# Kernel optimization log

Measured on AMD Instinct MI355X. Metric: run time of the kernel, lower is better.

Reference implementation:

```python
import jax, jax.numpy as jnp
import numpy as np
from jax import lax

B, T, N, H, NC = 2, 8, 512, 64, 10
NEG = -1e9
LN_EPS = 1e-5


def _gatv2(x, mask, Wl, Wr, att, b):
    # GATv2Conv (PyG semantics, eval mode): e_ij = att . leaky_relu(Wr x_i + Wl x_j),
    # softmax over source nodes j with self-loops, out_i = sum_j alpha_ij * (Wl x_j).
    # x: (B, N, Fin); mask: (N, N) bool adjacency incl. self-loops; att: (heads, C).
    heads, C = att.shape
    Bn, Nn, _ = x.shape
    xl = (x @ Wl).reshape(Bn, Nn, heads, C)  # source transform
    xr = (x @ Wr).reshape(Bn, Nn, heads, C)  # target transform
    s = jax.nn.leaky_relu(xr[:, :, None] + xl[:, None, :], 0.2)  # (B, Ni, Nj, h, C)
    e = jnp.einsum('bijhc,hc->bijh', s, att)
    e = jnp.where(mask[None, :, :, None], e, NEG)
    alpha = jax.nn.softmax(e, axis=2)  # softmax over neighbors j
    out = jnp.einsum('bijh,bjhc->bihc', alpha, xl)
    return out.reshape(Bn, Nn, heads * C) + b


def _gru_layer(x, Wih, Whh, bih, bhh):
    # torch nn.GRU single layer, batch_first; x: (B, T, Hin)
    h0 = jnp.zeros((x.shape[0], Whh.shape[0]), x.dtype)
    def step(h, xt):
        gi = xt @ Wih + bih
        gh = h @ Whh + bhh
        ir, iz, inn = jnp.split(gi, 3, axis=-1)
        hr, hz, hn = jnp.split(gh, 3, axis=-1)
        r = jax.nn.sigmoid(ir + hr)
        z = jax.nn.sigmoid(iz + hz)
        n = jnp.tanh(inn + r * hn)
        hnew = (1.0 - z) * n + z * h
        return hnew, hnew
    _, ys = lax.scan(step, h0, jnp.swapaxes(x, 0, 1))
    return jnp.swapaxes(ys, 0, 1)


def setup_inputs() -> dict:
    key = jax.random.key(0)
    ks = jax.random.split(key, 20)
    def rn(i, shape, s=0.1):
        return jax.random.normal(ks[i], shape, jnp.float32) * s
    x_seq = jax.random.normal(ks[0], (B, T, N, 1), jnp.float32)
    a = jax.random.uniform(ks[1], (N, N))
    up = jnp.triu((a > 0.95).astype(jnp.float32), 1)
    static_adj = up + up.T  # sparse symmetric 0/1 static graph
    dyn_W = jax.random.normal(ks[2], (N, N), jnp.float32)
    reg_lambda = jnp.array([0.05], jnp.float32)
    return {
        'x_seq': x_seq, 'static_adj': static_adj, 'dyn_W': dyn_W, 'reg_lambda': reg_lambda,
        'g1_Wl': rn(3, (1, H)), 'g1_Wr': rn(4, (1, H)), 'g1_att': rn(5, (4, H // 4)), 'g1_b': jnp.zeros(H),
        'g2_Wl': rn(6, (H, H)), 'g2_Wr': rn(7, (H, H)), 'g2_att': rn(8, (1, H)), 'g2_b': jnp.zeros(H),
        'gru_Wih0': rn(9, (H, 3 * H)), 'gru_Whh0': rn(10, (H, 3 * H)), 'gru_bih0': jnp.zeros(3 * H), 'gru_bhh0': jnp.zeros(3 * H),
        'gru_Wih1': rn(11, (H, 3 * H)), 'gru_Whh1': rn(12, (H, 3 * H)), 'gru_bih1': jnp.zeros(3 * H), 'gru_bhh1': jnp.zeros(3 * H),
        'attn_W': rn(13, (H, 1)), 'attn_b': jnp.zeros(1),
        'cls_W1': rn(14, (H, H)), 'cls_b1': jnp.zeros(H), 'ln_g': jnp.ones(H), 'ln_b': jnp.zeros(H),
        'cls_W2': rn(15, (H, NC)), 'cls_b2': jnp.zeros(NC),
    }


def reference(x_seq, static_adj, dyn_W, reg_lambda,
              g1_Wl, g1_Wr, g1_att, g1_b, g2_Wl, g2_Wr, g2_att, g2_b,
              gru_Wih0, gru_Whh0, gru_bih0, gru_bhh0,
              gru_Wih1, gru_Whh1, gru_bih1, gru_bhh1,
              attn_W, attn_b, cls_W1, cls_b1, ln_g, ln_b, cls_W2, cls_b2):
    Bn, Tn, Nn, _ = x_seq.shape
    lam = jnp.maximum(reg_lambda[0], 0.01)
    t = jnp.arange(Tn, dtype=x_seq.dtype)
    gts = jnp.exp(-lam * t)  # gating values per timestep
    dyn = jax.nn.relu(dyn_W + dyn_W.T)
    fused = gts[:, None, None] * static_adj + (1.0 - gts)[:, None, None] * dyn  # (T, N, N)
    masks = (fused > 0) | jnp.eye(Nn, dtype=bool)[None]  # edge set + self-loops

    def step(carry, inp):
        xt, mask = inp  # xt: (B, N, 1)
        h = jax.nn.elu(_gatv2(xt, mask, g1_Wl, g1_Wr, g1_att, g1_b))
        h = jax.nn.elu(_gatv2(h, mask, g2_Wl, g2_Wr, g2_att, g2_b))
        return carry, h.mean(axis=1)  # (B, H) graph readout

    _, reps = lax.scan(step, 0.0, (jnp.swapaxes(x_seq, 0, 1), masks))
    h_seq = jnp.swapaxes(reps, 0, 1)  # (B, T, H)

    gru_out = _gru_layer(h_seq, gru_Wih0, gru_Whh0, gru_bih0, gru_bhh0)
    gru_out = _gru_layer(gru_out, gru_Wih1, gru_Whh1, gru_bih1, gru_bhh1)

    att_scores = jax.nn.softmax((gru_out @ attn_W + attn_b)[..., 0], axis=1)  # (B, T)
    final = jnp.einsum('bt,bth->bh', att_scores, gru_out)

    z = final @ cls_W1 + cls_b1
    mu = jnp.mean(z, axis=-1, keepdims=True)
    var = jnp.var(z, axis=-1, keepdims=True)
    z = (z - mu) / jnp.sqrt(var + LN_EPS) * ln_g + ln_b
    z = jax.nn.gelu(z, approximate=False)
    logits = z @ cls_W2 + cls_b2
    return logits, gts, att_scores
```

## Files before the change

kernel.cpp:

```cpp
#include <hip/hip_runtime.h>
#include <math.h>

#define BB 2
#define TT 8
#define NN 512
#define HH 64
#define NC 10

typedef unsigned char uchar;

__device__ __forceinline__ float elu1(float v){ return v > 0.f ? v : expm1f(v); }
__device__ __forceinline__ float sigm(float v){ return 1.f/(1.f+expf(-v)); }

__global__ __launch_bounds__(256) void k_mask(
    const float* __restrict__ dW, const float* __restrict__ sadj,
    uchar* __restrict__ M0, uchar* __restrict__ M1,
    float* __restrict__ Z2, float* __restrict__ hseq,
    const float* __restrict__ att1, const float* __restrict__ Wr1,
    const float* __restrict__ Wl1, float* __restrict__ AB,
    const float* __restrict__ Whh0, const float* __restrict__ Wih1,
    const float* __restrict__ Whh1, float4* __restrict__ WT4)
{
    __shared__ float tr[64][65];
    int bx = blockIdx.x, by = blockIdx.y;
    int tid = threadIdx.x;
    if (blockIdx.z == 1){
        int idx = (by*8 + bx)*256 + tid;
        if (idx < 3*4096){
            int m = idx >> 12, r = idx & 4095;
            int gg = r >> 6, k = r & 63;
            const float* W = (m == 0) ? Whh0 : (m == 1) ? Wih1 : Whh1;
            float4 o;
            o.x = W[k*192 + gg];
            o.y = W[k*192 + 64 + gg];
            o.z = W[k*192 + 128 + gg];
            o.w = 0.f;
            WT4[(size_t)m*4096 + r] = o;
        }
        return;
    }
    int i0 = by*64, j0 = bx*64;
    #pragma unroll
    for (int q = 0; q < 4; ++q){
        int r = (tid >> 4) + 16*q, c4 = tid & 15;
        float4 v = *(const float4*)&dW[(size_t)(j0+r)*NN + i0 + 4*c4];
        tr[r][4*c4+0] = v.x; tr[r][4*c4+1] = v.y;
        tr[r][4*c4+2] = v.z; tr[r][4*c4+3] = v.w;
    }
    __syncthreads();
    #pragma unroll
    for (int q = 0; q < 4; ++q){
        int row = (tid >> 4) + 16*q, c4 = tid & 15;
        int i = i0 + row, j = j0 + 4*c4;
        float4 d  = *(const float4*)&dW[(size_t)i*NN + j];
        float4 sa = *(const float4*)&sadj[(size_t)i*NN + j];
        uchar4 m0, m1;
        float dd0 = d.x + tr[4*c4+0][row];
        float dd1 = d.y + tr[4*c4+1][row];
        float dd2 = d.z + tr[4*c4+2][row];
        float dd3 = d.w + tr[4*c4+3][row];
        m0.x = (sa.x > 0.f) || (i == j+0);
        m0.y = (sa.y > 0.f) || (i == j+1);
        m0.z = (sa.z > 0.f) || (i == j+2);
        m0.w = (sa.w > 0.f) || (i == j+3);
        m1.x = m0.x || (dd0 > 0.f);
        m1.y = m0.y || (dd1 > 0.f);
        m1.z = m0.z || (dd2 > 0.f);
        m1.w = m0.w || (dd3 > 0.f);
        *(uchar4*)&M0[(size_t)i*NN + j] = m0;
        *(uchar4*)&M1[(size_t)i*NN + j] = m1;
    }
    int flat = (by*8 + bx)*256 + tid;
    if (flat < BB*TT*NN) Z2[flat] = 0.f;
    else if (flat < BB*TT*NN + BB*TT*HH) hseq[flat - BB*TT*NN] = 0.f;
    if (bx == 0 && by == 0 && tid < 8){
        int h = tid & 3;
        const float* W = (tid < 4) ? Wr1 : Wl1;
        float s = 0.f;
        for (int c = 0; c < 16; ++c) s += att1[h*16+c]*W[h*16+c];
        AB[tid] = s;
    }
}

__global__ __launch_bounds__(256) void k_gat1f(
    const float* __restrict__ x_seq, const uchar* __restrict__ M0,
    const uchar* __restrict__ M1,
    const float* __restrict__ Wl, const float* __restrict__ Wr,
    const float* __restrict__ att, const float* __restrict__ bias,
    const float* __restrict__ AB,
    const float* __restrict__ Wl2, const float* __restrict__ Wr2,
    const float* __restrict__ att2,
    float* __restrict__ xl2, float* __restrict__ xr2,
    float* __restrict__ ui, float* __restrict__ vj)
{
    __shared__ float x_s[NN];
    __shared__ float S_s[4][4];
    __shared__ float h_s[4][HH];
    __shared__ float Wl2_s[64*64];
    __shared__ float Wr2_s[64*64];
    int bt = blockIdx.y; int t = bt % TT;
    int i0 = blockIdx.x * 4;
    int tid = threadIdx.x;
    int il = tid >> 6, jl = tid & 63;
    int i = i0 + il;
    const uchar* M = t ? M1 : M0;
    ((float2*)x_s)[tid] = ((const float2*)(x_seq + bt*NN))[tid];
    #pragma unroll
    for (int q = 0; q < 4; ++q){
        int idx = q*256 + tid;
        ((float4*)Wl2_s)[idx] = ((const float4*)Wl2)[idx];
        ((float4*)Wr2_s)[idx] = ((const float4*)Wr2)[idx];
    }
    __syncthreads();
    float xi = x_s[i];
    const uchar* Mrow = M + (size_t)i*NN;
    float xj[8], msk[8];
    #pragma unroll
    for (int jj = 0; jj < 8; ++jj){
        int j = jj*64 + jl;
        xj[jj] = x_s[j];
        msk[jj] = Mrow[j] ? 1.f : 0.f;
    }
    float sw[4] = {0,0,0,0}, swx[4] = {0,0,0,0};
    for (int h = 0; h < 4; ++h){
        float acc[8] = {0,0,0,0,0,0,0,0};
        #pragma unroll
        for (int c = 0; c < 16; ++c){
            int hc = h*16 + c;
            float wl = Wl[hc];
            float q  = 0.4f * att[hc];
            float pr = xi * Wr[hc];
            #pragma unroll
            for (int jj = 0; jj < 8; ++jj){
                float s = fmaf(xj[jj], wl, pr);
                acc[jj] = fmaf(q, fabsf(s), acc[jj]);
            }
        }
        float lin = 0.6f * xi * AB[h];
        float al6 = 0.6f * AB[4+h];
        #pragma unroll
        for (int jj = 0; jj < 8; ++jj){
            float e = acc[jj] + fmaf(al6, xj[jj], lin);
            float w = msk[jj] * __expf(e);
            sw[h] += w;
            swx[h] = fmaf(w, xj[jj], swx[h]);
        }
    }
    #pragma unroll
    for (int off = 32; off; off >>= 1){
        #pragma unroll
        for (int h = 0; h < 4; ++h){
            sw[h]  += __shfl_down(sw[h],  off);
            swx[h] += __shfl_down(swx[h], off);
        }
    }
    if (jl == 0){
        #pragma unroll
        for (int h = 0; h < 4; ++h) S_s[il][h] = swx[h] / sw[h];
    }
    __syncthreads();
    {
        int hc = tid & 63, row = tid >> 6;
        float v = S_s[row][hc >> 4] * Wl[hc] + bias[hc];
        h_s[row][hc] = elu1(v);
    }
    __syncthreads();
    {
        int c = tid & 63, row = tid >> 6;
        float al = 0.f, ar = 0.f;
        #pragma unroll 8
        for (int k = 0; k < 64; ++k){
            float hv = h_s[row][k];
            al = fmaf(hv, Wl2_s[k*64 + c], al);
            ar = fmaf(hv, Wr2_s[k*64 + c], ar);
        }
        size_t ridx = (size_t)(bt*NN + i0 + row);
        xl2[ridx*HH + c] = al;
        xr2[ridx*HH + c] = ar;
        float a2 = att2[c];
        float pu = a2 * ar, pv = a2 * al;
        #pragma unroll
        for (int off = 32; off; off >>= 1){
            pu += __shfl_down(pu, off);
            pv += __shfl_down(pv, off);
        }
        if (c == 0){ ui[ridx] = pu; vj[ridx] = pv; }
    }
}

__global__ __launch_bounds__(256) void k_e2(
    const float* __restrict__ xl2, const float* __restrict__ xr2,
    const uchar* __restrict__ M0, const uchar* __restrict__ M1,
    const float* __restrict__ att,
    const float* __restrict__ ui, const float* __restrict__ vj,
    float* __restrict__ WgT, float* __restrict__ Z2)
{
    __shared__ float xrT[64][68];
    __shared__ float xlT[64][68];
    int bt = blockIdx.z, t = bt % TT;
    int i0 = blockIdx.y*64, j0 = blockIdx.x*64;
    int base = bt*NN;
    int tid = threadIdx.x;
    const uchar* M = t ? M1 : M0;
    {
        int r = tid >> 2;
        #pragma unroll
        for (int q = 0; q < 4; ++q){
            int c4 = (tid & 3) + 4*q;
            float4 a = *(const float4*)&xr2[(size_t)(base+i0+r)*HH + 4*c4];
            float4 b = *(const float4*)&xl2[(size_t)(base+j0+r)*HH + 4*c4];
            xrT[4*c4+0][r] = a.x; xrT[4*c4+1][r] = a.y;
            xrT[4*c4+2][r] = a.z; xrT[4*c4+3][r] = a.w;
            xlT[4*c4+0][r] = b.x; xlT[4*c4+1][r] = b.y;
            xlT[4*c4+2][r] = b.z; xlT[4*c4+3][r] = b.w;
        }
    }
    int ti = tid >> 4, tj = tid & 15;
    int iL = ti*4, jL = tj*4;
    float4 u4 = *(const float4*)&ui[base+i0+iL];
    float4 v4 = *(const float4*)&vj[base+j0+jL];
    float uu[4] = {u4.x, u4.y, u4.z, u4.w};
    float vv[4] = {v4.x, v4.y, v4.z, v4.w};
    float acc[4][4];
    #pragma unroll
    for (int ii = 0; ii < 4; ++ii)
        #pragma unroll
        for (int jj = 0; jj < 4; ++jj)
            acc[ii][jj] = 0.6f*(uu[ii] + vv[jj]);
    __syncthreads();
    #pragma unroll 8
    for (int c = 0; c < 64; ++c){
        float qa = 0.4f * att[c];
        float4 a4 = *(const float4*)&xrT[c][iL];
        float4 b4 = *(const float4*)&xlT[c][jL];
        float a[4] = {a4.x, a4.y, a4.z, a4.w};
        float b[4] = {b4.x, b4.y, b4.z, b4.w};
        #pragma unroll
        for (int ii = 0; ii < 4; ++ii)
            #pragma unroll
            for (int jj = 0; jj < 4; ++jj)
                acc[ii][jj] = fmaf(qa, fabsf(a[ii] + b[jj]), acc[ii][jj]);
    }
    float w[4][4];
    #pragma unroll
    for (int ii = 0; ii < 4; ++ii){
        int i = i0 + iL + ii;
        uchar4 mr = *(const uchar4*)&M[(size_t)i*NN + j0 + jL];
        w[ii][0] = mr.x ? __expf(acc[ii][0]) : 0.f;
        w[ii][1] = mr.y ? __expf(acc[ii][1]) : 0.f;
        w[ii][2] = mr.z ? __expf(acc[ii][2]) : 0.f;
        w[ii][3] = mr.w ? __expf(acc[ii][3]) : 0.f;
    }
    #pragma unroll
    for (int jj = 0; jj < 4; ++jj){
        int j = j0 + jL + jj;
        float4 wv = { w[0][jj], w[1][jj], w[2][jj], w[3][jj] };
        *(float4*)&WgT[(size_t)(base+j)*NN + i0 + iL] = wv;
    }
    #pragma unroll
    for (int ii = 0; ii < 4; ++ii){
        float zi = w[ii][0] + w[ii][1] + w[ii][2] + w[ii][3];
        zi += __shfl_down(zi, 8);
        zi += __shfl_down(zi, 4);
        zi += __shfl_down(zi, 2);
        zi += __shfl_down(zi, 1);
        if (tj == 0) atomicAdd(&Z2[base + i0 + iL + ii], zi);
    }
}

__global__ __launch_bounds__(256) void k_a2(
    const float* __restrict__ WgT, const float* __restrict__ xl2,
    const float* __restrict__ Z2, const float* __restrict__ bias,
    float* __restrict__ hseq)
{
    __shared__ float a_s[64][20];
    __shared__ float x_s[64][68];
    __shared__ float msum[64];
    int bt = blockIdx.y;
    int i0 = blockIdx.x * 16;
    int base = bt * NN;
    int tid = threadIdx.x;
    int tg = tid >> 4, tc = tid & 15;
    if (tid < 64) msum[tid] = 0.f;
    float4 acc = {0,0,0,0};
    for (int jc = 0; jc < 8; ++jc){
        int j0 = jc*64;
        {
            int row = tid >> 2, c4 = tid & 3;
            ((float4*)&a_s[row][0])[c4] = ((const float4*)&WgT[(size_t)(base+j0+row)*NN + i0])[c4];
        }
        #pragma unroll
        for (int q = 0; q < 4; ++q){
            int idx = q*256 + tid; int row = idx >> 4, c4 = idx & 15;
            ((float4*)&x_s[row][0])[c4] = ((const float4*)&xl2[(size_t)(base+j0+row)*HH])[c4];
        }
        __syncthreads();
        #pragma unroll 8
        for (int j = 0; j < 64; ++j){
            float a = a_s[j][tg];
            float4 xv = ((float4*)&x_s[j][0])[tc];
            acc.x = fmaf(a, xv.x, acc.x);
            acc.y = fmaf(a, xv.y, acc.y);
            acc.z = fmaf(a, xv.z, acc.z);
            acc.w = fmaf(a, xv.w, acc.w);
        }
        __syncthreads();
    }
    float rz = 1.f / Z2[base + i0 + tg];
    float4 b4 = ((const float4*)bias)[tc];
    float4 h;
    h.x = elu1(acc.x*rz + b4.x);
    h.y = elu1(acc.y*rz + b4.y);
    h.z = elu1(acc.z*rz + b4.z);
    h.w = elu1(acc.w*rz + b4.w);
    atomicAdd(&msum[tc*4+0], h.x);
    atomicAdd(&msum[tc*4+1], h.y);
    atomicAdd(&msum[tc*4+2], h.z);
    atomicAdd(&msum[tc*4+3], h.w);
    __syncthreads();
    if (tid < 64) atomicAdd(&hseq[bt*HH + tid], msum[tid]*(1.f/(float)NN));
}

__global__ __launch_bounds__(256) void k_pre(
    const float* __restrict__ hseq, const float* __restrict__ Wih0,
    const float* __restrict__ bih0, float* __restrict__ gi0)
{
    int idx = blockIdx.x*256 + threadIdx.x;
    int bt = idx / 192, g = idx % 192;
    const float* x = hseq + bt*HH;
    float acc = bih0[g];
    #pragma unroll 8
    for (int k = 0; k < HH; ++k)
        acc = fmaf(x[k], Wih0[k*192 + g], acc);
    gi0[idx] = acc;
}

#define P4 65
__global__ __launch_bounds__(512) void k_gru2(
    const float* __restrict__ gi0, const float4* __restrict__ WT4,
    const float* __restrict__ bhh0,
    const float* __restrict__ bih1, const float* __restrict__ bhh1,
    const float* __restrict__ lamp, const float* __restrict__ attn_W,
    const float* __restrict__ attn_b, const float* __restrict__ W1,
    const float* __restrict__ b1, const float* __restrict__ ln_g,
    const float* __restrict__ ln_b, const float* __restrict__ W2,
    const float* __restrict__ b2, float* __restrict__ out)
{
    __shared__ float4 WA[64*P4];
    __shared__ float4 WB[64*P4];
    __shared__ float gi_s[BB*TT*192];
    __shared__ float y_s[BB*TT*HH];
    __shared__ float sc_s[BB][TT], at_s[BB][TT];
    __shared__ float fin_s[BB][HH], z_s[BB][HH], g_s[BB][HH];
    __shared__ float mu_s[BB], iv_s[BB];
    int tid = threadIdx.x;
    int wave = tid >> 6, lane = tid & 63;
    for (int v = tid; v < 4096; v += 512){
        WA[(v >> 6)*P4 + (v & 63)] = WT4[v];
        WB[(v >> 6)*P4 + (v & 63)] = WT4[4096 + v];
    }
    for (int v = tid; v < BB*TT*192; v += 512) gi_s[v] = gi0[v];
    __syncthreads();
    float y[TT];
    float g1r[TT], g1z[TT], g1n[TT];
    if (wave < 2){
        int b = wave;
        float bhr = bhh0[lane], bhz = bhh0[64+lane], bhn = bhh0[128+lane];
        float h = 0.f;
        for (int t = 0; t < TT; ++t){
            float ghr = bhr, ghz = bhz, ghn = bhn;
            #pragma unroll 16
            for (int k = 0; k < 64; ++k){
                float4 w4 = WA[lane*P4 + k];
                float hk = __shfl(h, k);
                ghr = fmaf(w4.x, hk, ghr);
                ghz = fmaf(w4.y, hk, ghz);
                ghn = fmaf(w4.z, hk, ghn);
            }
            const float* gi = &gi_s[(b*TT + t)*192];
            float r = sigm(gi[lane] + ghr);
            float z = sigm(gi[64+lane] + ghz);
            float n = tanhf(gi[128+lane] + r*ghn);
            h = (1.f - z)*n + z*h;
            y[t] = h;
        }
        float bi1r = bih1[lane], bi1z = bih1[64+lane], bi1n = bih1[128+lane];
        #pragma unroll
        for (int t = 0; t < TT; ++t){ g1r[t] = bi1r; g1z[t] = bi1z; g1n[t] = bi1n; }
        #pragma unroll 8
        for (int k = 0; k < 64; ++k){
            float4 w4 = WB[lane*P4 + k];
            #pragma unroll
            for (int t = 0; t < TT; ++t){
                float yk = __shfl(y[t], k);
                g1r[t] = fmaf(w4.x, yk, g1r[t]);
                g1z[t] = fmaf(w4.y, yk, g1z[t]);
                g1n[t] = fmaf(w4.z, yk, g1n[t]);
            }
        }
    }
    __syncthreads();
    if (wave >= 2){
        for (int v = tid - 128; v < 4096; v += 384)
            WA[(v >> 6)*P4 + (v & 63)] = WT4[2*4096 + v];
    }
    __syncthreads();
    if (wave < 2){
        int b = wave;
        float bhr = bhh1[lane], bhz = bhh1[64+lane], bhn = bhh1[128+lane];
        float h = 0.f;
        for (int t = 0; t < TT; ++t){
            float ghr = bhr, ghz = bhz, ghn = bhn;
            #pragma unroll 16
            for (int k = 0; k < 64; ++k){
                float4 w4 = WA[lane*P4 + k];
                float hk = __shfl(h, k);
                ghr = fmaf(w4.x, hk, ghr);
                ghz = fmaf(w4.y, hk, ghz);
                ghn = fmaf(w4.z, hk, ghn);
            }
            float r = sigm(g1r[t] + ghr);
            float z = sigm(g1z[t] + ghz);
            float n = tanhf(g1n[t] + r*ghn);
            h = (1.f - z)*n + z*h;
            y_s[(b*TT + t)*HH + lane] = h;
        }
    }
    __syncthreads();
    float lam = fmaxf(lamp[0], 0.01f);
    if (tid < TT) out[BB*NC + tid] = expf(-lam*(float)tid);
    if (tid < BB*TT){
        int bb = tid >> 3, t = tid & 7;
        float s = attn_b[0];
        const float* r = &y_s[(bb*TT+t)*HH];
        for (int h = 0; h < HH; ++h) s += r[h]*attn_W[h];
        sc_s[bb][t] = s;
    }
    __syncthreads();
    if (tid < BB){
        float mx = -INFINITY;
        for (int t = 0; t < TT; ++t) mx = fmaxf(mx, sc_s[tid][t]);
        float se = 0.f;
        for (int t = 0; t < TT; ++t){ float w = expf(sc_s[tid][t]-mx); at_s[tid][t] = w; se += w; }
        for (int t = 0; t < TT; ++t){
            at_s[tid][t] /= se;
            out[BB*NC + TT + tid*TT + t] = at_s[tid][t];
        }
    }
    __syncthreads();
    if (tid < BB*HH){
        int bb = tid >> 6, h = tid & 63;
        float a = 0.f;
        for (int t = 0; t < TT; ++t) a += at_s[bb][t]*y_s[(bb*TT+t)*HH + h];
        fin_s[bb][h] = a;
    }
    __syncthreads();
    if (tid < BB*HH){
        int bb = tid >> 6, h = tid & 63;
        float a = b1[h];
        for (int k = 0; k < HH; ++k) a += fin_s[bb][k]*W1[k*HH+h];
        z_s[bb][h] = a;
    }
    __syncthreads();
    if (tid < BB){
        float mu = 0.f;
        for (int h = 0; h < HH; ++h) mu += z_s[tid][h];
        mu *= (1.f/HH);
        float v = 0.f;
        for (int h = 0; h < HH; ++h){ float d = z_s[tid][h]-mu; v += d*d; }
        v *= (1.f/HH);
        mu_s[tid] = mu; iv_s[tid] = 1.f/sqrtf(v + 1e-5f);
    }
    __syncthreads();
    if (tid < BB*HH){
        int bb = tid >> 6, h = tid & 63;
        float zn = (z_s[bb][h]-mu_s[bb])*iv_s[bb]*ln_g[h] + ln_b[h];
        g_s[bb][h] = 0.5f*zn*(1.f + erff(zn*0.70710678118654752f));
    }
    __syncthreads();
    if (tid < BB*NC){
        int bb = tid / NC, c = tid % NC;
        float a = b2[c];
        for (int k = 0; k < HH; ++k) a += g_s[bb][k]*W2[k*NC+c];
        out[bb*NC + c] = a;
    }
}

extern "C" void kernel_launch(void* const* d_in, const int* in_sizes, int n_in,
                              void* d_out, int out_size, void* d_ws, size_t ws_size,
                              hipStream_t stream)
{
    const float* x_seq = (const float*)d_in[0];
    const float* sadj  = (const float*)d_in[1];
    const float* dynW  = (const float*)d_in[2];
    const float* lamp  = (const float*)d_in[3];
    const float* g1_Wl = (const float*)d_in[4];
    const float* g1_Wr = (const float*)d_in[5];
    const float* g1_att= (const float*)d_in[6];
    const float* g1_b  = (const float*)d_in[7];
    const float* g2_Wl = (const float*)d_in[8];
    const float* g2_Wr = (const float*)d_in[9];
    const float* g2_att= (const float*)d_in[10];
    const float* g2_b  = (const float*)d_in[11];
    const float* Wih0  = (const float*)d_in[12];
    const float* Whh0  = (const float*)d_in[13];
    const float* bih0  = (const float*)d_in[14];
    const float* bhh0  = (const float*)d_in[15];
    const float* Wih1  = (const float*)d_in[16];
    const float* Whh1  = (const float*)d_in[17];
    const float* bih1  = (const float*)d_in[18];
    const float* bhh1  = (const float*)d_in[19];
    const float* attnW = (const float*)d_in[20];
    const float* attnb = (const float*)d_in[21];
    const float* W1    = (const float*)d_in[22];
    const float* b1    = (const float*)d_in[23];
    const float* lng   = (const float*)d_in[24];
    const float* lnb   = (const float*)d_in[25];
    const float* W2    = (const float*)d_in[26];
    const float* b2    = (const float*)d_in[27];
    float* out = (float*)d_out;

    const int RWS = BB*TT*NN*HH;
    uchar* M0 = (uchar*)d_ws;
    uchar* M1 = M0 + (size_t)NN*NN;
    float* fb = (float*)(M1 + (size_t)NN*NN);
    float* Z2   = fb;
    float* AB   = Z2   + BB*TT*NN;
    float* ui   = AB   + 16;
    float* vj   = ui   + BB*TT*NN;
    float* xl2  = vj   + BB*TT*NN;
    float* xr2  = xl2  + RWS;
    float* WgT  = xr2  + RWS;
    float* hseq = WgT  + (size_t)BB*TT*NN*NN;
    float* gi0  = hseq + BB*TT*HH;
    float4* WT4 = (float4*)(gi0 + BB*TT*192);

    k_mask <<<dim3(8,8,2), 256, 0, stream>>>(dynW, sadj, M0, M1, Z2, hseq, g1_att, g1_Wr, g1_Wl, AB,
                                             Whh0, Wih1, Whh1, WT4);
    k_gat1f<<<dim3(NN/4, BB*TT), 256, 0, stream>>>(x_seq, M0, M1, g1_Wl, g1_Wr, g1_att, g1_b, AB,
                                                   g2_Wl, g2_Wr, g2_att, xl2, xr2, ui, vj);
    k_e2   <<<dim3(NN/64, NN/64, BB*TT), 256, 0, stream>>>(xl2, xr2, M0, M1, g2_att, ui, vj, WgT, Z2);
    k_a2   <<<dim3(NN/16, BB*TT), 256, 0, stream>>>(WgT, xl2, Z2, g2_b, hseq);
    k_pre  <<<12, 256, 0, stream>>>(hseq, Wih0, bih0, gi0);
    k_gru2 <<<1, 512, 0, stream>>>(gi0, WT4, bhh0, bih1, bhh1,
                                   lamp, attnW, attnb, W1, b1, lng, lnb, W2, b2, out);
}
```

Before: 223.0 us.

## Fuse GAT2 scores, aggregation and GRU tail into one flash-style kernel

Replaces the separate edge-score kernel (which wrote a full B*T*N*N weight matrix to global memory), the aggregation kernel, the gi0 precompute and the single-block GRU kernel with one flash-style kernel. Each block computes scores for 8 target rows against 64-column source tiles held in swizzled shared memory, aggregates immediately, and keeps the softmax denominator locally. The last block to finish, detected through an atomic counter, runs the input projection, both GRU layers and the classifier, reading GRU weights straight from global memory instead of staging them in LDS. This removes the large intermediate traffic and several launches, at the cost of less register tiling per score, a serialized tail inside the final block and reliance on a grid-wide atomic handoff.

New measurement: 330.3 us. 1.48x slower.

```diff
diff --git a/kernel.cpp b/kernel.cpp
--- a/kernel.cpp
+++ b/kernel.cpp
@@ -15,7 +15,7 @@
 __global__ __launch_bounds__(256) void k_mask(
     const float* __restrict__ dW, const float* __restrict__ sadj,
     uchar* __restrict__ M0, uchar* __restrict__ M1,
-    float* __restrict__ Z2, float* __restrict__ hseq,
+    float* __restrict__ hseq, unsigned* __restrict__ done,
     const float* __restrict__ att1, const float* __restrict__ Wr1,
     const float* __restrict__ Wl1, float* __restrict__ AB,
     const float* __restrict__ Whh0, const float* __restrict__ Wih1,
@@ -35,7 +35,7 @@
             o.y = W[k*192 + 64 + gg];
             o.z = W[k*192 + 128 + gg];
             o.w = 0.f;
-            WT4[(size_t)m*4096 + r] = o;
+            WT4[idx] = o;
         }
         return;
     }
@@ -71,8 +71,8 @@
         *(uchar4*)&M1[(size_t)i*NN + j] = m1;
     }
     int flat = (by*8 + bx)*256 + tid;
-    if (flat < BB*TT*NN) Z2[flat] = 0.f;
-    else if (flat < BB*TT*NN + BB*TT*HH) hseq[flat - BB*TT*NN] = 0.f;
+    if (flat < BB*TT*HH) hseq[flat] = 0.f;
+    else if (flat == BB*TT*HH) done[0] = 0u;
     if (bx == 0 && by == 0 && tid < 8){
         int h = tid & 3;
         const float* W = (tid < 4) ? Wr1 : Wl1;
@@ -188,157 +188,15 @@
     }
 }
 
-__global__ __launch_bounds__(256) void k_e2(
+#define SWZ(c4, j) ((c4) ^ (((j) >> 3) & 3))
+__global__ __launch_bounds__(256) void k_flash2(
     const float* __restrict__ xl2, const float* __restrict__ xr2,
     const uchar* __restrict__ M0, const uchar* __restrict__ M1,
-    const float* __restrict__ att,
+    const float* __restrict__ att, const float* __restrict__ bias,
     const float* __restrict__ ui, const float* __restrict__ vj,
-    float* __restrict__ WgT, float* __restrict__ Z2)
-{
-    __shared__ float xrT[64][68];
-    __shared__ float xlT[64][68];
-    int bt = blockIdx.z, t = bt % TT;
-    int i0 = blockIdx.y*64, j0 = blockIdx.x*64;
-    int base = bt*NN;
-    int tid = threadIdx.x;
-    const uchar* M = t ? M1 : M0;
-    {
-        int r = tid >> 2;
-        #pragma unroll
-        for (int q = 0; q < 4; ++q){
-            int c4 = (tid & 3) + 4*q;
-            float4 a = *(const float4*)&xr2[(size_t)(base+i0+r)*HH + 4*c4];
-            float4 b = *(const float4*)&xl2[(size_t)(base+j0+r)*HH + 4*c4];
-            xrT[4*c4+0][r] = a.x; xrT[4*c4+1][r] = a.y;
-            xrT[4*c4+2][r] = a.z; xrT[4*c4+3][r] = a.w;
-            xlT[4*c4+0][r] = b.x; xlT[4*c4+1][r] = b.y;
-            xlT[4*c4+2][r] = b.z; xlT[4*c4+3][r] = b.w;
-        }
-    }
-    int ti = tid >> 4, tj = tid & 15;
-    int iL = ti*4, jL = tj*4;
-    float4 u4 = *(const float4*)&ui[base+i0+iL];
-    float4 v4 = *(const float4*)&vj[base+j0+jL];
-    float uu[4] = {u4.x, u4.y, u4.z, u4.w};
-    float vv[4] = {v4.x, v4.y, v4.z, v4.w};
-    float acc[4][4];
-    #pragma unroll
-    for (int ii = 0; ii < 4; ++ii)
-        #pragma unroll
-        for (int jj = 0; jj < 4; ++jj)
-            acc[ii][jj] = 0.6f*(uu[ii] + vv[jj]);
-    __syncthreads();
-    #pragma unroll 8
-    for (int c = 0; c < 64; ++c){
-        float qa = 0.4f * att[c];
-        float4 a4 = *(const float4*)&xrT[c][iL];
-        float4 b4 = *(const float4*)&xlT[c][jL];
-        float a[4] = {a4.x, a4.y, a4.z, a4.w};
-        float b[4] = {b4.x, b4.y, b4.z, b4.w};
-        #pragma unroll
-        for (int ii = 0; ii < 4; ++ii)
-            #pragma unroll
-            for (int jj = 0; jj < 4; ++jj)
-                acc[ii][jj] = fmaf(qa, fabsf(a[ii] + b[jj]), acc[ii][jj]);
-    }
-    float w[4][4];
-    #pragma unroll
-    for (int ii = 0; ii < 4; ++ii){
-        int i = i0 + iL + ii;
-        uchar4 mr = *(const uchar4*)&M[(size_t)i*NN + j0 + jL];
-        w[ii][0] = mr.x ? __expf(acc[ii][0]) : 0.f;
-        w[ii][1] = mr.y ? __expf(acc[ii][1]) : 0.f;
-        w[ii][2] = mr.z ? __expf(acc[ii][2]) : 0.f;
-        w[ii][3] = mr.w ? __expf(acc[ii][3]) : 0.f;
-    }
-    #pragma unroll
-    for (int jj = 0; jj < 4; ++jj){
-        int j = j0 + jL + jj;
-        float4 wv = { w[0][jj], w[1][jj], w[2][jj], w[3][jj] };
-        *(float4*)&WgT[(size_t)(base+j)*NN + i0 + iL] = wv;
-    }
-    #pragma unroll
-    for (int ii = 0; ii < 4; ++ii){
-        float zi = w[ii][0] + w[ii][1] + w[ii][2] + w[ii][3];
-        zi += __shfl_down(zi, 8);
-        zi += __shfl_down(zi, 4);
-        zi += __shfl_down(zi, 2);
-        zi += __shfl_down(zi, 1);
-        if (tj == 0) atomicAdd(&Z2[base + i0 + iL + ii], zi);
-    }
-}
-
-__global__ __launch_bounds__(256) void k_a2(
-    const float* __restrict__ WgT, const float* __restrict__ xl2,
-    const float* __restrict__ Z2, const float* __restrict__ bias,
-    float* __restrict__ hseq)
-{
-    __shared__ float a_s[64][20];
-    __shared__ float x_s[64][68];
-    __shared__ float msum[64];
-    int bt = blockIdx.y;
-    int i0 = blockIdx.x * 16;
-    int base = bt * NN;
-    int tid = threadIdx.x;
-    int tg = tid >> 4, tc = tid & 15;
-    if (tid < 64) msum[tid] = 0.f;
-    float4 acc = {0,0,0,0};
-    for (int jc = 0; jc < 8; ++jc){
-        int j0 = jc*64;
-        {
-            int row = tid >> 2, c4 = tid & 3;
-            ((float4*)&a_s[row][0])[c4] = ((const float4*)&WgT[(size_t)(base+j0+row)*NN + i0])[c4];
-        }
-        #pragma unroll
-        for (int q = 0; q < 4; ++q){
-            int idx = q*256 + tid; int row = idx >> 4, c4 = idx & 15;
-            ((float4*)&x_s[row][0])[c4] = ((const float4*)&xl2[(size_t)(base+j0+row)*HH])[c4];
-        }
-        __syncthreads();
-        #pragma unroll 8
-        for (int j = 0; j < 64; ++j){
-            float a = a_s[j][tg];
-            float4 xv = ((float4*)&x_s[j][0])[tc];
-            acc.x = fmaf(a, xv.x, acc.x);
-            acc.y = fmaf(a, xv.y, acc.y);
-            acc.z = fmaf(a, xv.z, acc.z);
-            acc.w = fmaf(a, xv.w, acc.w);
-        }
-        __syncthreads();
-    }
-    float rz = 1.f / Z2[base + i0 + tg];
-    float4 b4 = ((const float4*)bias)[tc];
-    float4 h;
-    h.x = elu1(acc.x*rz + b4.x);
-    h.y = elu1(acc.y*rz + b4.y);
-    h.z = elu1(acc.z*rz + b4.z);
-    h.w = elu1(acc.w*rz + b4.w);
-    atomicAdd(&msum[tc*4+0], h.x);
-    atomicAdd(&msum[tc*4+1], h.y);
-    atomicAdd(&msum[tc*4+2], h.z);
-    atomicAdd(&msum[tc*4+3], h.w);
-    __syncthreads();
-    if (tid < 64) atomicAdd(&hseq[bt*HH + tid], msum[tid]*(1.f/(float)NN));
-}
-
-__global__ __launch_bounds__(256) void k_pre(
-    const float* __restrict__ hseq, const float* __restrict__ Wih0,
-    const float* __restrict__ bih0, float* __restrict__ gi0)
-{
-    int idx = blockIdx.x*256 + threadIdx.x;
-    int bt = idx / 192, g = idx % 192;
-    const float* x = hseq + bt*HH;
-    float acc = bih0[g];
-    #pragma unroll 8
-    for (int k = 0; k < HH; ++k)
-        acc = fmaf(x[k], Wih0[k*192 + g], acc);
-    gi0[idx] = acc;
-}
-
-#define P4 65
-__global__ __launch_bounds__(512) void k_gru2(
-    const float* __restrict__ gi0, const float4* __restrict__ WT4,
-    const float* __restrict__ bhh0,
+    float* __restrict__ hseq, unsigned* __restrict__ done,
+    const float* __restrict__ Wih0, const float* __restrict__ bih0,
+    const float4* __restrict__ WT4, const float* __restrict__ bhh0,
     const float* __restrict__ bih1, const float* __restrict__ bhh1,
     const float* __restrict__ lamp, const float* __restrict__ attn_W,
     const float* __restrict__ attn_b, const float* __restrict__ W1,
@@ -346,142 +204,257 @@
     const float* __restrict__ ln_b, const float* __restrict__ W2,
     const float* __restrict__ b2, float* __restrict__ out)
 {
-    __shared__ float4 WA[64*P4];
-    __shared__ float4 WB[64*P4];
-    __shared__ float gi_s[BB*TT*192];
-    __shared__ float y_s[BB*TT*HH];
-    __shared__ float sc_s[BB][TT], at_s[BB][TT];
-    __shared__ float fin_s[BB][HH], z_s[BB][HH], g_s[BB][HH];
-    __shared__ float mu_s[BB], iv_s[BB];
+    __shared__ __align__(16) float S[5632];
+    __shared__ unsigned isLast;
+    float* xrR  = S;
+    float* xlR  = S + 544;
+    float* w_s  = S + 4896;
+    float* vj_s = S + 5440;
+    float* Zl   = S + 5504;
+    float* msum = S + 5512;
+    int bt = blockIdx.y, it = blockIdx.x;
+    int i0 = it*8, t = bt % TT, base = bt*NN;
+    const uchar* M = t ? M1 : M0;
     int tid = threadIdx.x;
+    int ti = tid >> 5, tj = tid & 31;
+    int tc = tj & 15, jh = tj >> 4;
+    if (tid < 128){
+        int r = tid >> 4, c4 = tid & 15;
+        *(float4*)&xrR[r*68 + 4*c4] = *(const float4*)&xr2[(size_t)(base+i0+r)*HH + 4*c4];
+    }
+    if (tid < 64) msum[tid] = 0.f;
+    float u = ui[base + i0 + ti];
+    float zacc = 0.f;
+    float4 acc = {0,0,0,0};
+    int sa = (tj >> 3) & 3;
+    for (int jt = 0; jt < 8; ++jt){
+        int j0 = jt*64;
+        #pragma unroll
+        for (int q = 0; q < 4; ++q){
+            int idx = q*256 + tid;
+            int r = idx >> 4, c4 = idx & 15;
+            *(float4*)&xlR[r*68 + 4*SWZ(c4, r)] =
+                *(const float4*)&xl2[(size_t)(base+j0+r)*HH + 4*c4];
+        }
+        if (tid < 64) vj_s[tid] = vj[base + j0 + tid];
+        __syncthreads();
+        int ja = tj, jb = tj + 32;
+        float e0a = 0.6f*(u + vj_s[ja]), e0b = 0.f;
+        float e1a = 0.6f*(u + vj_s[jb]), e1b = 0.f;
+        #pragma unroll
+        for (int cq = 0; cq < 16; ++cq){
+            float4 qa = ((const float4*)att)[cq];
+            qa.x *= 0.4f; qa.y *= 0.4f; qa.z *= 0.4f; qa.w *= 0.4f;
+            float4 a4 = *(const float4*)&xrR[ti*68 + 4*cq];
+            float4 b0 = *(const float4*)&xlR[ja*68 + 4*(cq ^ sa)];
+            float4 b1 = *(const float4*)&xlR[jb*68 + 4*(cq ^ sa)];
+            e0a = fmaf(qa.x, fabsf(a4.x + b0.x), e0a);
+            e0b = fmaf(qa.y, fabsf(a4.y + b0.y), e0b);
+            e0a = fmaf(qa.z, fabsf(a4.z + b0.z), e0a);
+            e0b = fmaf(qa.w, fabsf(a4.w + b0.w), e0b);
+            e1a = fmaf(qa.x, fabsf(a4.x + b1.x), e1a);
+            e1b = fmaf(qa.y, fabsf(a4.y + b1.y), e1b);
+            e1a = fmaf(qa.z, fabsf(a4.z + b1.z), e1a);
+            e1b = fmaf(qa.w, fabsf(a4.w + b1.w), e1b);
+        }
+        const uchar* Mrow = M + (size_t)(i0+ti)*NN + j0;
+        float w0 = Mrow[ja] ? __expf(e0a + e0b) : 0.f;
+        float w1 = Mrow[jb] ? __expf(e1a + e1b) : 0.f;
+        w_s[ti*68 + ja] = w0;
+        w_s[ti*68 + jb] = w1;
+        float zp = w0 + w1;
+        zp += __shfl_down(zp, 16, 32);
+        zp += __shfl_down(zp, 8, 32);
+        zp += __shfl_down(zp, 4, 32);
+        zp += __shfl_down(zp, 2, 32);
+        zp += __shfl_down(zp, 1, 32);
+        if (tj == 0) zacc += zp;
+        __syncthreads();
+        #pragma unroll 8
+        for (int jj = 0; jj < 32; ++jj){
+            int j = jh*32 + jj;
+            float w = w_s[ti*68 + j];
+            float4 x4 = *(const float4*)&xlR[j*68 + 4*SWZ(tc, j)];
+            acc.x = fmaf(w, x4.x, acc.x);
+            acc.y = fmaf(w, x4.y, acc.y);
+            acc.z = fmaf(w, x4.z, acc.z);
+            acc.w = fmaf(w, x4.w, acc.w);
+        }
+        __syncthreads();
+    }
+    acc.x += __shfl_down(acc.x, 16, 32);
+    acc.y += __shfl_down(acc.y, 16, 32);
+    acc.z += __shfl_down(acc.z, 16, 32);
+    acc.w += __shfl_down(acc.w, 16, 32);
+    if (tj == 0) Zl[ti] = zacc;
+    __syncthreads();
+    if (jh == 0){
+        float rz = 1.f / Zl[ti];
+        float4 b4 = ((const float4*)bias)[tc];
+        float4 h;
+        h.x = elu1(acc.x*rz + b4.x);
+        h.y = elu1(acc.y*rz + b4.y);
+        h.z = elu1(acc.z*rz + b4.z);
+        h.w = elu1(acc.w*rz + b4.w);
+        atomicAdd(&msum[4*tc+0], h.x);
+        atomicAdd(&msum[4*tc+1], h.y);
+        atomicAdd(&msum[4*tc+2], h.z);
+        atomicAdd(&msum[4*tc+3], h.w);
+    }
+    __syncthreads();
+    if (tid < 64) atomicAdd(&hseq[bt*HH + tid], msum[tid]*(1.f/(float)NN));
+    if (tid == 0){
+        __threadfence();
+        unsigned old = __hip_atomic_fetch_add(done, 1u, __ATOMIC_ACQ_REL, __HIP_MEMORY_SCOPE_AGENT);
+        isLast = (old == 64u*16u - 1u) ? 1u : 0u;
+        if (isLast) __threadfence();
+    }
+    __syncthreads();
+    if (!isLast) return;
+    float* hs   = S;
+    float* gi_s = S + 1024;
+    float* y_s  = S + 4096;
+    float* sc_s = S + 5120;
+    float* at_s = S + 5136;
+    float* fin_s= S + 5152;
+    float* z_s  = S + 5280;
+    float* g_s  = S + 5408;
+    float* mu_s = S + 5536;
+    float* iv_s = S + 5538;
+    __syncthreads();
+    for (int o = tid; o < BB*TT*HH; o += 256)
+        hs[o] = __hip_atomic_load(&hseq[o], __ATOMIC_RELAXED, __HIP_MEMORY_SCOPE_AGENT);
+    __syncthreads();
+    for (int o = tid; o < BB*TT*192; o += 256){
+        int b = o / 192, g = o % 192;
+        float a = bih0[g];
+        #pragma unroll 8
+        for (int k = 0; k < HH; ++k)
+            a = fmaf(hs[b*HH + k], Wih0[k*192 + g], a);
+        gi_s[o] = a;
+    }
+    __syncthreads();
     int wave = tid >> 6, lane = tid & 63;
-    for (int v = tid; v < 4096; v += 512){
-        WA[(v >> 6)*P4 + (v & 63)] = WT4[v];
-        WB[(v >> 6)*P4 + (v & 63)] = WT4[4096 + v];
-    }
-    for (int v = tid; v < BB*TT*192; v += 512) gi_s[v] = gi0[v];
-    __syncthreads();
-    float y[TT];
-    float g1r[TT], g1z[TT], g1n[TT];
     if (wave < 2){
         int b = wave;
-        float bhr = bhh0[lane], bhz = bhh0[64+lane], bhn = bhh0[128+lane];
-        float h = 0.f;
-        for (int t = 0; t < TT; ++t){
-            float ghr = bhr, ghz = bhz, ghn = bhn;
-            #pragma unroll 16
+        float y[TT], g1r[TT], g1z[TT], g1n[TT];
+        {
+            float bhr = bhh0[lane], bhz = bhh0[64+lane], bhn = bhh0[128+lane];
+            float h = 0.f;
+            for (int tt = 0; tt < TT; ++tt){
+                float ghr = bhr, ghz = bhz, ghn = bhn;
+                #pragma unroll
+                for (int k = 0; k < 64; ++k){
+                    float4 w4 = WT4[lane*64 + k];
+                    float hk = __shfl(h, k);
+                    ghr = fmaf(w4.x, hk, ghr);
+                    ghz = fmaf(w4.y, hk, ghz);
+                    ghn = fmaf(w4.z, hk, ghn);
+                }
+                const float* gi = &gi_s[(b*TT + tt)*192];
+                float r = sigm(gi[lane] + ghr);
+                float z = sigm(gi[64+lane] + ghz);
+                float n = tanhf(gi[128+lane] + r*ghn);
+                h = (1.f - z)*n + z*h;
+                y[tt] = h;
+            }
+        }
+        {
+            float bi1r = bih1[lane], bi1z = bih1[64+lane], bi1n = bih1[128+lane];
+            #pragma unroll
+            for (int tt = 0; tt < TT; ++tt){ g1r[tt] = bi1r; g1z[tt] = bi1z; g1n[tt] = bi1n; }
+            #pragma unroll 8
             for (int k = 0; k < 64; ++k){
-                float4 w4 = WA[lane*P4 + k];
-                float hk = __shfl(h, k);
-                ghr = fmaf(w4.x, hk, ghr);
-                ghz = fmaf(w4.y, hk, ghz);
-                ghn = fmaf(w4.z, hk, ghn);
+                float4 w4 = WT4[4096 + lane*64 + k];
+                #pragma unroll
+                for (int tt = 0; tt < TT; ++tt){
+                    float yk = __shfl(y[tt], k);
+                    g1r[tt] = fmaf(w4.x, yk, g1r[tt]);
+                    g1z[tt] = fmaf(w4.y, yk, g1z[tt]);
+                    g1n[tt] = fmaf(w4.z, yk, g1n[tt]);
+                }
             }
-            const float* gi = &gi_s[(b*TT + t)*192];
-            float r = sigm(gi[lane] + ghr);
-            float z = sigm(gi[64+lane] + ghz);
-            float n = tanhf(gi[128+lane] + r*ghn);
-            h = (1.f - z)*n + z*h;
-            y[t] = h;
-        }
-        float bi1r = bih1[lane], bi1z = bih1[64+lane], bi1n = bih1[128+lane];
-        #pragma unroll
-        for (int t = 0; t < TT; ++t){ g1r[t] = bi1r; g1z[t] = bi1z; g1n[t] = bi1n; }
-        #pragma unroll 8
-        for (int k = 0; k < 64; ++k){
-            float4 w4 = WB[lane*P4 + k];
-            #pragma unroll
-            for (int t = 0; t < TT; ++t){
-                float yk = __shfl(y[t], k);
-                g1r[t] = fmaf(w4.x, yk, g1r[t]);
-                g1z[t] = fmaf(w4.y, yk, g1z[t]);
-                g1n[t] = fmaf(w4.z, yk, g1n[t]);
+        }
+        {
+            float bhr = bhh1[lane], bhz = bhh1[64+lane], bhn = bhh1[128+lane];
+            float h = 0.f;
+            for (int tt = 0; tt < TT; ++tt){
+                float ghr = bhr, ghz = bhz, ghn = bhn;
+                #pragma unroll
+                for (int k = 0; k < 64; ++k){
+                    float4 w4 = WT4[2*4096 + lane*64 + k];
+                    float hk = __shfl(h, k);
+                    ghr = fmaf(w4.x, hk, ghr);
+                    ghz = fmaf(w4.y, hk, ghz);
+                    ghn = fmaf(w4.z, hk, ghn);
+                }
+                float r = sigm(g1r[tt] + ghr);
+                float z = sigm(g1z[tt] + ghz);
+                float n = tanhf(g1n[tt] + r*ghn);
+                h = (1.f - z)*n + z*h;
+                y_s[(b*TT + tt)*HH + lane] = h;
             }
-        }
-    }
-    __syncthreads();
-    if (wave >= 2){
-        for (int v = tid - 128; v < 4096; v += 384)
-            WA[(v >> 6)*P4 + (v & 63)] = WT4[2*4096 + v];
-    }
-    __syncthreads();
-    if (wave < 2){
-        int b = wave;
-        float bhr = bhh1[lane], bhz = bhh1[64+lane], bhn = bhh1[128+lane];
-        float h = 0.f;
-        for (int t = 0; t < TT; ++t){
-            float ghr = bhr, ghz = bhz, ghn = bhn;
-            #pragma unroll 16
-            for (int k = 0; k < 64; ++k){
-                float4 w4 = WA[lane*P4 + k];
-                float hk = __shfl(h, k);
-                ghr = fmaf(w4.x, hk, ghr);
-                ghz = fmaf(w4.y, hk, ghz);
-                ghn = fmaf(w4.z, hk, ghn);
-            }
-            float r = sigm(g1r[t] + ghr);
-            float z = sigm(g1z[t] + ghz);
-            float n = tanhf(g1n[t] + r*ghn);
-            h = (1.f - z)*n + z*h;
-            y_s[(b*TT + t)*HH + lane] = h;
         }
     }
     __syncthreads();
     float lam = fmaxf(lamp[0], 0.01f);
     if (tid < TT) out[BB*NC + tid] = expf(-lam*(float)tid);
     if (tid < BB*TT){
-        int bb = tid >> 3, t = tid & 7;
+        int bb = tid >> 3, tt = tid & 7;
         float s = attn_b[0];
-        const float* r = &y_s[(bb*TT+t)*HH];
+        const float* r = &y_s[(bb*TT+tt)*HH];
         for (int h = 0; h < HH; ++h) s += r[h]*attn_W[h];
-        sc_s[bb][t] = s;
+        sc_s[bb*TT + tt] = s;
     }
     __syncthreads();
     if (tid < BB){
         float mx = -INFINITY;
-        for (int t = 0; t < TT; ++t) mx = fmaxf(mx, sc_s[tid][t]);
+        for (int tt = 0; tt < TT; ++tt) mx = fmaxf(mx, sc_s[tid*TT + tt]);
         float se = 0.f;
-        for (int t = 0; t < TT; ++t){ float w = expf(sc_s[tid][t]-mx); at_s[tid][t] = w; se += w; }
-        for (int t = 0; t < TT; ++t){
-            at_s[tid][t] /= se;
-            out[BB*NC + TT + tid*TT + t] = at_s[tid][t];
+        for (int tt = 0; tt < TT; ++tt){
+            float w = expf(sc_s[tid*TT + tt] - mx);
+            at_s[tid*TT + tt] = w; se += w;
+        }
+        for (int tt = 0; tt < TT; ++tt){
+            at_s[tid*TT + tt] /= se;
+            out[BB*NC + TT + tid*TT + tt] = at_s[tid*TT + tt];
         }
     }
     __syncthreads();
     if (tid < BB*HH){
         int bb = tid >> 6, h = tid & 63;
         float a = 0.f;
-        for (int t = 0; t < TT; ++t) a += at_s[bb][t]*y_s[(bb*TT+t)*HH + h];
-        fin_s[bb][h] = a;
+        for (int tt = 0; tt < TT; ++tt) a += at_s[bb*TT + tt]*y_s[(bb*TT+tt)*HH + h];
+        fin_s[bb*HH + h] = a;
     }
     __syncthreads();
     if (tid < BB*HH){
         int bb = tid >> 6, h = tid & 63;
         float a = b1[h];
-        for (int k = 0; k < HH; ++k) a += fin_s[bb][k]*W1[k*HH+h];
-        z_s[bb][h] = a;
+        for (int k = 0; k < HH; ++k) a += fin_s[bb*HH + k]*W1[k*HH+h];
+        z_s[bb*HH + h] = a;
     }
     __syncthreads();
     if (tid < BB){
         float mu = 0.f;
-        for (int h = 0; h < HH; ++h) mu += z_s[tid][h];
+        for (int h = 0; h < HH; ++h) mu += z_s[tid*HH + h];
         mu *= (1.f/HH);
         float v = 0.f;
-        for (int h = 0; h < HH; ++h){ float d = z_s[tid][h]-mu; v += d*d; }
+        for (int h = 0; h < HH; ++h){ float d = z_s[tid*HH + h]-mu; v += d*d; }
         v *= (1.f/HH);
         mu_s[tid] = mu; iv_s[tid] = 1.f/sqrtf(v + 1e-5f);
     }
     __syncthreads();
     if (tid < BB*HH){
         int bb = tid >> 6, h = tid & 63;
-        float zn = (z_s[bb][h]-mu_s[bb])*iv_s[bb]*ln_g[h] + ln_b[h];
-        g_s[bb][h] = 0.5f*zn*(1.f + erff(zn*0.70710678118654752f));
+        float zn = (z_s[bb*HH + h]-mu_s[bb])*iv_s[bb]*ln_g[h] + ln_b[h];
+        g_s[bb*HH + h] = 0.5f*zn*(1.f + erff(zn*0.70710678118654752f));
     }
     __syncthreads();
     if (tid < BB*NC){
         int bb = tid / NC, c = tid % NC;
         float a = b2[c];
-        for (int k = 0; k < HH; ++k) a += g_s[bb][k]*W2[k*NC+c];
+        for (int k = 0; k < HH; ++k) a += g_s[bb*HH + k]*W2[k*NC+c];
         out[bb*NC + c] = a;
     }
 }
@@ -524,24 +497,23 @@
     uchar* M0 = (uchar*)d_ws;
     uchar* M1 = M0 + (size_t)NN*NN;
     float* fb = (float*)(M1 + (size_t)NN*NN);
-    float* Z2   = fb;
-    float* AB   = Z2   + BB*TT*NN;
+    float* AB   = fb;
     float* ui   = AB   + 16;
     float* vj   = ui   + BB*TT*NN;
     float* xl2  = vj   + BB*TT*NN;
     float* xr2  = xl2  + RWS;
-    float* WgT  = xr2  + RWS;
-    float* hseq = WgT  + (size_t)BB*TT*NN*NN;
-    float* gi0  = hseq + BB*TT*HH;
-    float4* WT4 = (float4*)(gi0 + BB*TT*192);
-
-    k_mask <<<dim3(8,8,2), 256, 0, stream>>>(dynW, sadj, M0, M1, Z2, hseq, g1_att, g1_Wr, g1_Wl, AB,
-                                             Whh0, Wih1, Whh1, WT4);
-    k_gat1f<<<dim3(NN/4, BB*TT), 256, 0, stream>>>(x_seq, M0, M1, g1_Wl, g1_Wr, g1_att, g1_b, AB,
-                                                   g2_Wl, g2_Wr, g2_att, xl2, xr2, ui, vj);
-    k_e2   <<<dim3(NN/64, NN/64, BB*TT), 256, 0, stream>>>(xl2, xr2, M0, M1, g2_att, ui, vj, WgT, Z2);
-    k_a2   <<<dim3(NN/16, BB*TT), 256, 0, stream>>>(WgT, xl2, Z2, g2_b, hseq);
-    k_pre  <<<12, 256, 0, stream>>>(hseq, Wih0, bih0, gi0);
-    k_gru2 <<<1, 512, 0, stream>>>(gi0, WT4, bhh0, bih1, bhh1,
-                                   lamp, attnW, attnb, W1, b1, lng, lnb, W2, b2, out);
+    float* hseq = xr2  + RWS;
+    float* WT4  = hseq + BB*TT*HH;
+    unsigned* done = (unsigned*)(WT4 + 3*4096*4);
+
+    k_mask  <<<dim3(8,8,2), 256, 0, stream>>>(dynW, sadj, M0, M1, hseq, done,
+                                              g1_att, g1_Wr, g1_Wl, AB,
+                                              Whh0, Wih1, Whh1, (float4*)WT4);
+    k_gat1f <<<dim3(NN/4, BB*TT), 256, 0, stream>>>(x_seq, M0, M1, g1_Wl, g1_Wr, g1_att, g1_b, AB,
+                                                    g2_Wl, g2_Wr, g2_att, xl2, xr2, ui, vj);
+    k_flash2<<<dim3(NN/8, BB*TT), 256, 0, stream>>>(xl2, xr2, M0, M1, g2_att, g2_b, ui, vj,
+                                                    hseq, done,
+                                                    Wih0, bih0, (const float4*)WT4, bhh0,
+                                                    bih1, bhh1, lamp, attnW, attnb,
+                                                    W1, b1, lng, lnb, W2, b2, out);
 }
```
